# Performance work log

Measured on AMD Instinct MI355X. Metric: run time of the kernel, lower is better.

## Reference

```python
import jax, jax.numpy as jnp
import numpy as np

B = 16
L = 1024  # signal_length


def setup_inputs() -> dict:
    key = jax.random.key(0)
    ks = jax.random.split(key, 6)
    X = jax.random.normal(ks[0], (B, L), dtype=jnp.float32)
    # encoder projection Fc (the repo initializes it uniform(-0.5, 0.5))
    Fc = (jax.random.uniform(ks[1], (L, 2 * L), dtype=jnp.float32) - 0.5)
    # MLP weights (kaiming-ish scaling kept small for numerical sanity)
    W1 = jax.random.normal(ks[2], (2 * L, 50 * L), dtype=jnp.float32) * 0.02
    b1 = jax.random.normal(ks[3], (50 * L,), dtype=jnp.float32) * 0.02
    W2 = jax.random.normal(ks[4], (50 * L, 2 * L), dtype=jnp.float32) * 0.02
    b2 = jax.random.normal(ks[5], (2 * L,), dtype=jnp.float32) * 0.02
    return {"X": X, "Fc": Fc, "W1": W1, "b1": b1, "W2": W2, "b2": b2}


def _decode(z):
    # z: [B, 2L] -> reconstructed signal [B, L]
    yr = z[:, :L]
    yi = z[:, L:]
    amp = jnp.sqrt(yr * yr + yi * yi) / L          # [B, L]
    ph = jnp.arctan2(yi, yr)                        # [B, L]
    t = jnp.arange(L, dtype=jnp.float32)
    arg = (2.0 * jnp.pi / L) * (t[:, None] * t[None, :])  # [L(t), L(f)]
    # sinusoids[b, t, f] = amp[b, f] * cos(arg[t, f] + ph[b, f]); reduce over f
    sinusoids = amp[:, None, :] * jnp.cos(arg[None, :, :] + ph[:, None, :])
    return jnp.sum(sinusoids, axis=-1)              # [B, L]


def reference(X, Fc, W1, b1, W2, b2):
    y_pred = X @ Fc                                  # encoder: [B, 2L]
    h = jax.nn.sigmoid(y_pred @ W1 + b1)             # [B, 50L]
    z = h @ W2 + b2                                  # [B, 2L]
    return _decode(z)                                # [B, L]
```

## Files before the change

kernel.cpp:

```cpp
#include <hip/hip_runtime.h>
#include <math.h>

#define LL    1024
#define BB    16
#define NN1   2048
#define NNH   51200

using f32x2 = __attribute__((ext_vector_type(2))) float;

__global__ void k_xt(const float* __restrict__ X, float* __restrict__ XT) {
    int id = blockIdx.x * 256 + threadIdx.x;
    int n = id >> 4, b = id & 15;
    XT[id] = X[b * LL + n];
}

template <int CH, int NCOL>
__global__ __launch_bounds__(256, 4) void k_gpart(
        const float* __restrict__ AT,
        const float* __restrict__ W,
        float* __restrict__ part) {
    const int t  = threadIdx.x;
    const int n2 = blockIdx.x * 512 + t * 2;
    const int s  = blockIdx.y;
    const int m0 = s * CH;

    float2 acc[BB];
#pragma unroll
    for (int r = 0; r < BB; ++r) acc[r] = make_float2(0.f, 0.f);

    const float* wp = W  + (size_t)m0 * NCOL + n2;
    const float* ap = AT + (size_t)m0 * BB;
#pragma unroll 8
    for (int m = 0; m < CH; ++m) {
        const f32x2 w = __builtin_nontemporal_load((const f32x2*)wp);
        wp += NCOL;
        const float4 a0 = *(const float4*)(ap + 0);
        const float4 a1 = *(const float4*)(ap + 4);
        const float4 a2 = *(const float4*)(ap + 8);
        const float4 a3 = *(const float4*)(ap + 12);
        ap += BB;
        acc[ 0].x = fmaf(a0.x, w.x, acc[ 0].x);  acc[ 0].y = fmaf(a0.x, w.y, acc[ 0].y);
        acc[ 1].x = fmaf(a0.y, w.x, acc[ 1].x);  acc[ 1].y = fmaf(a0.y, w.y, acc[ 1].y);
        acc[ 2].x = fmaf(a0.z, w.x, acc[ 2].x);  acc[ 2].y = fmaf(a0.z, w.y, acc[ 2].y);
        acc[ 3].x = fmaf(a0.w, w.x, acc[ 3].x);  acc[ 3].y = fmaf(a0.w, w.y, acc[ 3].y);
        acc[ 4].x = fmaf(a1.x, w.x, acc[ 4].x);  acc[ 4].y = fmaf(a1.x, w.y, acc[ 4].y);
        acc[ 5].x = fmaf(a1.y, w.x, acc[ 5].x);  acc[ 5].y = fmaf(a1.y, w.y, acc[ 5].y);
        acc[ 6].x = fmaf(a1.z, w.x, acc[ 6].x);  acc[ 6].y = fmaf(a1.z, w.y, acc[ 6].y);
        acc[ 7].x = fmaf(a1.w, w.x, acc[ 7].x);  acc[ 7].y = fmaf(a1.w, w.y, acc[ 7].y);
        acc[ 8].x = fmaf(a2.x, w.x, acc[ 8].x);  acc[ 8].y = fmaf(a2.x, w.y, acc[ 8].y);
        acc[ 9].x = fmaf(a2.y, w.x, acc[ 9].x);  acc[ 9].y = fmaf(a2.y, w.y, acc[ 9].y);
        acc[10].x = fmaf(a2.z, w.x, acc[10].x);  acc[10].y = fmaf(a2.z, w.y, acc[10].y);
        acc[11].x = fmaf(a2.w, w.x, acc[11].x);  acc[11].y = fmaf(a2.w, w.y, acc[11].y);
        acc[12].x = fmaf(a3.x, w.x, acc[12].x);  acc[12].y = fmaf(a3.x, w.y, acc[12].y);
        acc[13].x = fmaf(a3.y, w.x, acc[13].x);  acc[13].y = fmaf(a3.y, w.y, acc[13].y);
        acc[14].x = fmaf(a3.z, w.x, acc[14].x);  acc[14].y = fmaf(a3.z, w.y, acc[14].y);
        acc[15].x = fmaf(a3.w, w.x, acc[15].x);  acc[15].y = fmaf(a3.w, w.y, acc[15].y);
    }

    float* pp = part + ((size_t)s * BB) * NCOL + n2;
#pragma unroll
    for (int r = 0; r < BB; ++r)
        *(float2*)(pp + (size_t)r * NCOL) = acc[r];
}

template <bool SIG>
__global__ __launch_bounds__(256) void k_redT(
        const float* __restrict__ part,
        const float* __restrict__ bias,
        float* __restrict__ outT,
        int N, int splits) {
    const int n = blockIdx.x * 256 + threadIdx.x;
    float acc[BB];
#pragma unroll
    for (int b = 0; b < BB; ++b) acc[b] = 0.f;
    for (int s = 0; s < splits; ++s) {
        const float* p = part + ((size_t)s * BB) * N + n;
#pragma unroll
        for (int b = 0; b < BB; ++b) acc[b] += p[(size_t)b * N];
    }
    const float bv = bias ? bias[n] : 0.f;
#pragma unroll
    for (int b = 0; b < BB; ++b) {
        float v = acc[b] + bv;
        if (SIG) v = 1.f / (1.f + __expf(-v));
        acc[b] = v;
    }
    float4* o = (float4*)(outT + (size_t)n * BB);
    o[0] = make_float4(acc[ 0], acc[ 1], acc[ 2], acc[ 3]);
    o[1] = make_float4(acc[ 4], acc[ 5], acc[ 6], acc[ 7]);
    o[2] = make_float4(acc[ 8], acc[ 9], acc[10], acc[11]);
    o[3] = make_float4(acc[12], acc[13], acc[14], acc[15]);
}

__global__ __launch_bounds__(256) void k_redN(
        const float* __restrict__ part,
        const float* __restrict__ bias,
        float* __restrict__ out,
        int splits) {
    const int id = blockIdx.x * 256 + threadIdx.x;
    const int n  = id & (NN1 - 1);
    float acc[4] = {0.f, 0.f, 0.f, 0.f};
#pragma unroll 8
    for (int s = 0; s < splits; ++s)
        acc[s & 3] += part[(size_t)s * (BB * NN1) + id];
    out[id] = (acc[0] + acc[1]) + (acc[2] + acc[3]) + bias[n];
}

__global__ __launch_bounds__(512) void k_decode(const float* __restrict__ z2,
                                                float* __restrict__ out) {
    __shared__ float yr[LL], yi[LL];
    const int t   = threadIdx.x;
    const int b   = blockIdx.y;
    const int i   = blockIdx.x * 256 + (t & 255);
    const int jh  = t >> 8;
    for (int j = t; j < LL; j += 512) {
        yr[j] = z2[b * NN1 + j];
        yi[j] = z2[b * NN1 + LL + j];
    }
    __syncthreads();
    float acc = 0.f;
    int r = (jh * 512 * i) & (LL - 1);
    for (int j = 0; j < 512; ++j) {
        float rev = (float)r * (1.0f / LL);
        float c = __builtin_amdgcn_cosf(rev);
        float s = __builtin_amdgcn_sinf(rev);
        acc = fmaf(yr[jh * 512 + j], c, acc);
        acc = fmaf(-yi[jh * 512 + j], s, acc);
        r = (r + i) & (LL - 1);
    }
    __shared__ float partial[256];
    if (jh == 1) partial[t & 255] = acc;
    __syncthreads();
    if (jh == 0) out[b * LL + i] = (acc + partial[t]) * (1.0f / LL);
}

extern "C" void kernel_launch(void* const* d_in, const int* in_sizes, int n_in,
                              void* d_out, int out_size, void* d_ws, size_t ws_size,
                              hipStream_t stream) {
    const float* X  = (const float*)d_in[0];
    const float* Fc = (const float*)d_in[1];
    const float* W1 = (const float*)d_in[2];
    const float* b1 = (const float*)d_in[3];
    const float* W2 = (const float*)d_in[4];
    const float* b2 = (const float*)d_in[5];
    float* out = (float*)d_out;

    float* ws     = (float*)d_ws;
    float* XT     = ws;
    float* ypredT = XT     + LL * BB;
    float* hT     = ypredT + NN1 * BB;
    float* z2     = hT     + NNH * BB;
    float* parts0 = z2     + BB * NN1;
    float* parts1 = parts0 + 16 * BB * NN1;
    float* parts2 = parts1 + 8 * BB * NNH;

    k_xt<<<dim3(LL * BB / 256), 256, 0, stream>>>(X, XT);
    k_gpart<64, NN1><<<dim3(NN1 / 512, 16), 256, 0, stream>>>(XT, Fc, parts0);
    k_redT<false><<<dim3(NN1 / 256), 256, 0, stream>>>(parts0, nullptr, ypredT, NN1, 16);
    k_gpart<256, NNH><<<dim3(NNH / 512, 8), 256, 0, stream>>>(ypredT, W1, parts1);
    k_redT<true><<<dim3(NNH / 256), 256, 0, stream>>>(parts1, b1, hT, NNH, 8);
    k_gpart<256, NN1><<<dim3(NN1 / 512, 200), 256, 0, stream>>>(hT, W2, parts2);
    k_redN<<<dim3(BB * NN1 / 256), 256, 0, stream>>>(parts2, b2, z2, 200);
    k_decode<<<dim3(LL / 256, BB), 512, 0, stream>>>(z2, out);
}
```

Measured before the change: 236.5 us.

## Shrink GEMV blocks to one wavefront, split reductions by batch, widen decode

```diff
diff --git a/kernel.cpp b/kernel.cpp
--- a/kernel.cpp
+++ b/kernel.cpp
@@ -15,12 +15,12 @@
 }
 
 template <int CH, int NCOL>
-__global__ __launch_bounds__(256, 4) void k_gpart(
+__global__ __launch_bounds__(64, 8) void k_gpart(
         const float* __restrict__ AT,
         const float* __restrict__ W,
         float* __restrict__ part) {
     const int t  = threadIdx.x;
-    const int n2 = blockIdx.x * 512 + t * 2;
+    const int n2 = blockIdx.x * 128 + t * 2;
     const int s  = blockIdx.y;
     const int m0 = s * CH;
 
@@ -69,27 +69,22 @@
         const float* __restrict__ bias,
         float* __restrict__ outT,
         int N, int splits) {
-    const int n = blockIdx.x * 256 + threadIdx.x;
-    float acc[BB];
+    const int n  = blockIdx.x * 256 + threadIdx.x;
+    const int b0 = blockIdx.y * 4;
+    float acc[4] = {0.f, 0.f, 0.f, 0.f};
+    for (int s = 0; s < splits; ++s) {
+        const float* p = part + ((size_t)s * BB + b0) * N + n;
 #pragma unroll
-    for (int b = 0; b < BB; ++b) acc[b] = 0.f;
-    for (int s = 0; s < splits; ++s) {
-        const float* p = part + ((size_t)s * BB) * N + n;
-#pragma unroll
-        for (int b = 0; b < BB; ++b) acc[b] += p[(size_t)b * N];
+        for (int j = 0; j < 4; ++j) acc[j] += p[(size_t)j * N];
     }
     const float bv = bias ? bias[n] : 0.f;
 #pragma unroll
-    for (int b = 0; b < BB; ++b) {
-        float v = acc[b] + bv;
+    for (int j = 0; j < 4; ++j) {
+        float v = acc[j] + bv;
         if (SIG) v = 1.f / (1.f + __expf(-v));
-        acc[b] = v;
+        acc[j] = v;
     }
-    float4* o = (float4*)(outT + (size_t)n * BB);
-    o[0] = make_float4(acc[ 0], acc[ 1], acc[ 2], acc[ 3]);
-    o[1] = make_float4(acc[ 4], acc[ 5], acc[ 6], acc[ 7]);
-    o[2] = make_float4(acc[ 8], acc[ 9], acc[10], acc[11]);
-    o[3] = make_float4(acc[12], acc[13], acc[14], acc[15]);
+    *(float4*)(outT + (size_t)n * BB + b0) = make_float4(acc[0], acc[1], acc[2], acc[3]);
 }
 
 __global__ __launch_bounds__(256) void k_redN(
@@ -106,32 +101,36 @@
     out[id] = (acc[0] + acc[1]) + (acc[2] + acc[3]) + bias[n];
 }
 
-__global__ __launch_bounds__(512) void k_decode(const float* __restrict__ z2,
-                                                float* __restrict__ out) {
+__global__ __launch_bounds__(1024) void k_decode(const float* __restrict__ z2,
+                                                 float* __restrict__ out) {
     __shared__ float yr[LL], yi[LL];
-    const int t   = threadIdx.x;
-    const int b   = blockIdx.y;
-    const int i   = blockIdx.x * 256 + (t & 255);
-    const int jh  = t >> 8;
-    for (int j = t; j < LL; j += 512) {
-        yr[j] = z2[b * NN1 + j];
-        yi[j] = z2[b * NN1 + LL + j];
+    __shared__ float partial[3 * 256];
+    const int t  = threadIdx.x;
+    const int b  = blockIdx.y;
+    const int il = t & 255;
+    const int i  = blockIdx.x * 256 + il;
+    const int jq = t >> 8;
+    if (t < LL) {
+        yr[t] = z2[b * NN1 + t];
+        yi[t] = z2[b * NN1 + LL + t];
     }
     __syncthreads();
     float acc = 0.f;
-    int r = (jh * 512 * i) & (LL - 1);
-    for (int j = 0; j < 512; ++j) {
+    int r = (jq * 256 * i) & (LL - 1);
+    const int j0 = jq * 256;
+    for (int jj = 0; jj < 256; ++jj) {
         float rev = (float)r * (1.0f / LL);
         float c = __builtin_amdgcn_cosf(rev);
         float s = __builtin_amdgcn_sinf(rev);
-        acc = fmaf(yr[jh * 512 + j], c, acc);
-        acc = fmaf(-yi[jh * 512 + j], s, acc);
+        acc = fmaf(yr[j0 + jj], c, acc);
+        acc = fmaf(-yi[j0 + jj], s, acc);
         r = (r + i) & (LL - 1);
     }
-    __shared__ float partial[256];
-    if (jh == 1) partial[t & 255] = acc;
+    if (jq > 0) partial[(jq - 1) * 256 + il] = acc;
     __syncthreads();
-    if (jh == 0) out[b * LL + i] = (acc + partial[t]) * (1.0f / LL);
+    if (jq == 0)
+        out[b * LL + i] = (acc + partial[il] + partial[256 + il] + partial[512 + il])
+                          * (1.0f / LL);
 }
 
 extern "C" void kernel_launch(void* const* d_in, const int* in_sizes, int n_in,
@@ -155,11 +154,11 @@
     float* parts2 = parts1 + 8 * BB * NNH;
 
     k_xt<<<dim3(LL * BB / 256), 256, 0, stream>>>(X, XT);
-    k_gpart<64, NN1><<<dim3(NN1 / 512, 16), 256, 0, stream>>>(XT, Fc, parts0);
-    k_redT<false><<<dim3(NN1 / 256), 256, 0, stream>>>(parts0, nullptr, ypredT, NN1, 16);
-    k_gpart<256, NNH><<<dim3(NNH / 512, 8), 256, 0, stream>>>(ypredT, W1, parts1);
-    k_redT<true><<<dim3(NNH / 256), 256, 0, stream>>>(parts1, b1, hT, NNH, 8);
-    k_gpart<256, NN1><<<dim3(NN1 / 512, 200), 256, 0, stream>>>(hT, W2, parts2);
-    k_redN<<<dim3(BB * NN1 / 256), 256, 0, stream>>>(parts2, b2, z2, 200);
-    k_decode<<<dim3(LL / 256, BB), 512, 0, stream>>>(z2, out);
+    k_gpart<64, NN1><<<dim3(NN1 / 128, 16), 64, 0, stream>>>(XT, Fc, parts0);
+    k_redT<false><<<dim3(NN1 / 256, 4), 256, 0, stream>>>(parts0, nullptr, ypredT, NN1, 16);
+    k_gpart<256, NNH><<<dim3(NNH / 128, 8), 64, 0, stream>>>(ypredT, W1, parts1);
+    k_redT<true><<<dim3(NNH / 256, 4), 256, 0, stream>>>(parts1, b1, hT, NNH, 8);
+    k_gpart<400, NN1><<<dim3(NN1 / 128, 128), 64, 0, stream>>>(hT, W2, parts2);
+    k_redN<<<dim3(BB * NN1 / 256), 256, 0, stream>>>(parts2, b2, z2, 128);
+    k_decode<<<dim3(LL / 256, BB), 1024, 0, stream>>>(z2, out);
 }
```

Result: slower. 258.3 us (+9.2%).
